# Kernel tuning notes

Measured on AMD Instinct MI355X. Metric: run time of the kernel, lower is better.

Reference implementation:

```python
import jax, jax.numpy as jnp
import numpy as np

NUM_Q = 8
DIM = 256
N_EMBED = 1024
COMMITMENT = 1.0


def setup_inputs() -> dict:
    key = jax.random.key(0)
    kx, ke = jax.random.split(key)
    x = jax.random.normal(kx, (32, 2048, DIM), dtype=jnp.float32)
    # one codebook per residual layer, stored as [dim, n_embed] like torch buffer `embed`
    embeds = jax.random.normal(ke, (NUM_Q, DIM, N_EMBED), dtype=jnp.float32)
    return {"x": x, "embeds": embeds}


def _vq_layer(residual, embed):
    # residual: [B, T, D]; embed: [D, K]
    flat = residual.reshape(-1, DIM)                                   # [N, D]
    dist = (jnp.sum(flat * flat, axis=1, keepdims=True)
            - 2.0 * flat @ embed
            + jnp.sum(embed * embed, axis=0, keepdims=True))           # [N, K]
    ind = jnp.argmin(dist, axis=1)                                     # [N]
    quantize = jnp.take(embed.T, ind, axis=0).reshape(residual.shape)  # [B, T, D]
    # commitment loss: mse(stopgrad(quantize), input)
    loss = jnp.mean((jax.lax.stop_gradient(quantize) - residual) ** 2) * COMMITMENT
    # straight-through estimator
    quantize_st = residual + jax.lax.stop_gradient(quantize - residual)
    # perplexity from code usage histogram
    counts = jnp.zeros((N_EMBED,), dtype=flat.dtype).at[ind].add(1.0)
    avg_probs = counts / flat.shape[0]
    perplexity = jnp.exp(-jnp.sum(avg_probs * jnp.log(avg_probs + 1e-10)))
    return quantize_st, loss, perplexity


def reference(x, embeds):
    def step(carry, embed):
        residual, quantized_out = carry
        q, loss, perp = _vq_layer(residual, embed)
        return (residual - q, quantized_out + q), (loss, perp)

    init = (x, jnp.zeros_like(x))
    (residual, quantized_out), (losses, perps) = jax.lax.scan(step, init, embeds)
    return quantized_out, losses, perps
```

## Files before the change

### kernel.cpp

```cpp
#include <hip/hip_runtime.h>
#include <math.h>
#include <stdint.h>

#define NQ 8
#define DIMV 256
#define KCODES 1024
#define NTOK 65536
#define NELEM (NTOK * DIMV)
#define TOKPB 64

typedef _Float16 f16x8 __attribute__((ext_vector_type(8)));
typedef float    f32x16 __attribute__((ext_vector_type(16)));

__device__ __forceinline__ int rotl3(int s) { return ((s << 3) | (s >> 2)) & 31; }

__global__ __launch_bounds__(256)
void vq_transpose(const float* __restrict__ embeds, float* __restrict__ embedT) {
    const int idx = blockIdx.x * 256 + threadIdx.x;
    const int q   = idx >> 18;
    const int rem = idx & 262143;
    const int k   = rem >> 8;
    const int d   = rem & 255;
    embedT[idx] = embeds[q * 262144 + d * 1024 + k];
}

__global__ __launch_bounds__(256)
void vq_e2(const float* __restrict__ embeds, float* __restrict__ e2) {
    const int idx = blockIdx.x * 256 + threadIdx.x;
    const int q = idx >> 10;
    const int k = idx & 1023;
    const float* e = embeds + q * 262144 + k;
    float s = 0.f;
    for (int d = 0; d < DIMV; ++d) {
        const float v = e[d * 1024];
        s += v * v;
    }
    e2[idx] = s;
}

__global__ __launch_bounds__(256)
void vq_embedB(const float* __restrict__ embeds, _Float16* __restrict__ embedB) {
    const int idx = blockIdx.x * 256 + threadIdx.x;
    const int j    = idx & 7;
    const int s    = (idx >> 3) & 127;
    const int part = (idx >> 10) & 1;
    const int w    = (idx >> 11) & 15;
    const int c    = (idx >> 15) & 15;
    const int q    = idx >> 19;
    const int h  = s >> 6;
    const int cl = s & 63;
    const int d  = c * 16 + h * 8 + j;
    const int k  = w * 64 + cl;
    const float v = embeds[q * 262144 + d * 1024 + k];
    const _Float16 hi = (_Float16)v;
    embedB[idx] = (part == 0) ? hi : (_Float16)(v - (float)hi);
}

#define LDS_BYTES 78272

__global__ __launch_bounds__(1024)
void vq_fused(const float* __restrict__ x, float* __restrict__ out,
              const float* __restrict__ embedT, const float* __restrict__ e2,
              const _Float16* __restrict__ embedB,
              float* __restrict__ lossSum, int* __restrict__ counts) {
    extern __shared__ char smem[];
    _Float16* Ahi = (_Float16*)smem;
    _Float16* Alo = (_Float16*)(smem + 32768);
    float* bestS   = (float*)(smem + 65536);
    int*   bestI   = (int*)(smem + 69696);
    int*   indF    = (int*)(smem + 73856);
    float* lossRed = (float*)(smem + 74112);
    float* e2Lds   = (float*)(smem + 74176);

    const int tid    = threadIdx.x;
    const int wave   = tid >> 6;
    const int lane   = tid & 63;
    const int l32    = lane & 31;
    const int h32    = lane >> 5;
    const int tok0   = blockIdx.x * TOKPB;
    const int codeBase = wave * 64;

#pragma unroll
    for (int k = 0; k < 2; ++k) {
        const int si = tid + k * 1024;
        const int t  = si >> 5;
        const int s  = si & 31;
        const float4 v0 = *(const float4*)(x + (tok0 + t) * 256 + s * 8);
        const float4 v1 = *(const float4*)(x + (tok0 + t) * 256 + s * 8 + 4);
        const float vv[8] = {v0.x, v0.y, v0.z, v0.w, v1.x, v1.y, v1.z, v1.w};
        f16x8 h8, l8;
#pragma unroll
        for (int e = 0; e < 8; ++e) {
            const _Float16 hi = (_Float16)vv[e];
            h8[e] = hi;
            l8[e] = (_Float16)(vv[e] - (float)hi);
        }
        const int ss = rotl3(s) ^ (t & 31);
        ((f16x8*)(Ahi + t * 256))[ss] = h8;
        ((f16x8*)(Alo + t * 256))[ss] = l8;
    }

#pragma unroll 1
    for (int q = 0; q < NQ; ++q) {
        const _Float16* embedBq = embedB + q * 524288;
        const float*    embedTq = embedT + q * (KCODES * DIMV);

        e2Lds[tid] = e2[q * KCODES + tid];
        __syncthreads();

        const char* gBw = (const char*)embedBq + wave * 4096 + h32 * 1024 + l32 * 16;

        float bsv0 = 3.4e38f, bsv1 = 3.4e38f;
        int   biv0 = 0x7fffffff, biv1 = 0x7fffffff;

#pragma unroll
        for (int pass = 0; pass < 2; ++pass) {
            f32x16 acc[2];
#pragma unroll
            for (int tt = 0; tt < 2; ++tt)
#pragma unroll
                for (int r = 0; r < 16; ++r) acc[tt][r] = 0.f;

            const char* gBp = gBw + pass * 512;

            f16x8 bH[3], bL[3];
            bH[0] = *(const f16x8*)(gBp);
            bL[0] = *(const f16x8*)(gBp + 2048);
            bH[1] = *(const f16x8*)(gBp + 65536);
            bL[1] = *(const f16x8*)(gBp + 65536 + 2048);

#pragma unroll
            for (int c = 0; c < 16; ++c) {
                const int cs = c % 3;
                if (c < 14) {
                    const char* gBn = gBp + (c + 2) * 65536;
                    bH[(c + 2) % 3] = *(const f16x8*)(gBn);
                    bL[(c + 2) % 3] = *(const f16x8*)(gBn + 2048);
                }
                f16x8 aH[2], aL[2];
#pragma unroll
                for (int tt = 0; tt < 2; ++tt) {
                    const int t  = tt * 32 + l32;
                    const int ss = rotl3(2 * c + h32) ^ l32;
                    aH[tt] = ((const f16x8*)(Ahi + t * 256))[ss];
                    aL[tt] = ((const f16x8*)(Alo + t * 256))[ss];
                }
#pragma unroll
                for (int tt = 0; tt < 2; ++tt) {
                    acc[tt] = __builtin_amdgcn_mfma_f32_32x32x16_f16(
                        bH[cs], aH[tt], acc[tt], 0, 0, 0);
                    acc[tt] = __builtin_amdgcn_mfma_f32_32x32x16_f16(
                        bL[cs], aH[tt], acc[tt], 0, 0, 0);
                    acc[tt] = __builtin_amdgcn_mfma_f32_32x32x16_f16(
                        bH[cs], aL[tt], acc[tt], 0, 0, 0);
                }
            }

#pragma unroll
            for (int tt = 0; tt < 2; ++tt) {
                float bs = (tt == 0) ? bsv0 : bsv1;
                int   bi = (tt == 0) ? biv0 : biv1;
#pragma unroll
                for (int r = 0; r < 16; ++r) {
                    const int cd = codeBase + pass * 32 + (r & 3) + 8 * (r >> 2) + 4 * h32;
                    const float sc = e2Lds[cd] - 2.0f * acc[tt][r];
                    if (sc < bs || (sc == bs && cd < bi)) { bs = sc; bi = cd; }
                }
                if (tt == 0) { bsv0 = bs; biv0 = bi; } else { bsv1 = bs; biv1 = bi; }
            }
        }

#pragma unroll
        for (int tt = 0; tt < 2; ++tt) {
            float bs = (tt == 0) ? bsv0 : bsv1;
            int   bi = (tt == 0) ? biv0 : biv1;
            const float so = __shfl_xor(bs, 32);
            const int   io = __shfl_xor(bi, 32);
            if (so < bs || (so == bs && io < bi)) { bs = so; bi = io; }
            if (h32 == 0) {
                bestS[wave * 65 + tt * 32 + l32] = bs;
                bestI[wave * 65 + tt * 32 + l32] = bi;
            }
        }
        __syncthreads();

        if (tid < 256) {
            const int t = tid >> 2;
            const int g = tid & 3;
            float bs = 3.4e38f;
            int   bi = 0x7fffffff;
#pragma unroll
            for (int i = 0; i < 4; ++i) {
                const int w = g * 4 + i;
                const float s2 = bestS[w * 65 + t];
                const int   i2 = bestI[w * 65 + t];
                if (s2 < bs || (s2 == bs && i2 < bi)) { bs = s2; bi = i2; }
            }
#pragma unroll
            for (int m = 1; m < 4; m <<= 1) {
                const float so = __shfl_xor(bs, m);
                const int   io = __shfl_xor(bi, m);
                if (so < bs || (so == bs && io < bi)) { bs = so; bi = io; }
            }
            if (g == 0) {
                indF[t] = bi;
                atomicAdd(&counts[q * KCODES + bi], 1);
            }
        }
        __syncthreads();

        {
            const int tl = tid >> 4;
            const int sg = tid & 15;
            const int csel = indF[tl];
            const float* gq = embedTq + csel * 256 + sg * 16;
            float lp = 0.f;
            f16x8* rowH = (f16x8*)(Ahi + tl * 256);
            f16x8* rowL = (f16x8*)(Alo + tl * 256);
#pragma unroll
            for (int it = 0; it < 2; ++it) {
                const int slot = rotl3(sg * 2 + it) ^ (tl & 31);
                f16x8 h8 = rowH[slot];
                f16x8 l8 = rowL[slot];
                const float4 q0 = *(const float4*)(gq + it * 8);
                const float4 q1 = *(const float4*)(gq + it * 8 + 4);
                const float qv[8] = {q0.x, q0.y, q0.z, q0.w, q1.x, q1.y, q1.z, q1.w};
#pragma unroll
                for (int e = 0; e < 8; ++e) {
                    const float rv = (float)h8[e] + (float)l8[e];
                    const float nr = rv - qv[e];
                    lp += nr * nr;
                    const _Float16 nh = (_Float16)nr;
                    h8[e] = nh;
                    l8[e] = (_Float16)(nr - (float)nh);
                }
                rowH[slot] = h8;
                rowL[slot] = l8;
            }
#pragma unroll
            for (int off = 32; off > 0; off >>= 1) lp += __shfl_down(lp, off);
            if (lane == 0) lossRed[wave] = lp;
        }
        __syncthreads();
        if (tid < 64) {
            float v = (lane < 16) ? lossRed[lane] : 0.f;
#pragma unroll
            for (int off = 8; off > 0; off >>= 1) v += __shfl_down(v, off);
            if (lane == 0) atomicAdd(lossSum + q, v);
        }
    }

#pragma unroll
    for (int k = 0; k < 2; ++k) {
        const int si = tid + k * 1024;
        const int t  = si >> 5;
        const int s  = si & 31;
        const int ss = rotl3(s) ^ (t & 31);
        const f16x8 h8 = ((const f16x8*)(Ahi + t * 256))[ss];
        const f16x8 l8 = ((const f16x8*)(Alo + t * 256))[ss];
        const float4 x0 = *(const float4*)(x + (tok0 + t) * 256 + s * 8);
        const float4 x1 = *(const float4*)(x + (tok0 + t) * 256 + s * 8 + 4);
        float4 o0, o1;
        o0.x = x0.x - ((float)h8[0] + (float)l8[0]);
        o0.y = x0.y - ((float)h8[1] + (float)l8[1]);
        o0.z = x0.z - ((float)h8[2] + (float)l8[2]);
        o0.w = x0.w - ((float)h8[3] + (float)l8[3]);
        o1.x = x1.x - ((float)h8[4] + (float)l8[4]);
        o1.y = x1.y - ((float)h8[5] + (float)l8[5]);
        o1.z = x1.z - ((float)h8[6] + (float)l8[6]);
        o1.w = x1.w - ((float)h8[7] + (float)l8[7]);
        *(float4*)(out + (tok0 + t) * 256 + s * 8)     = o0;
        *(float4*)(out + (tok0 + t) * 256 + s * 8 + 4) = o1;
    }
}

__global__ __launch_bounds__(256)
void vq_finalize(const int* __restrict__ counts, const float* __restrict__ lossSum,
                 float* __restrict__ outTail) {
    const int q = blockIdx.x;
    const int tid = threadIdx.x;
    float s = 0.f;
    for (int k = tid; k < KCODES; k += 256) {
        const float p = (float)counts[q * KCODES + k] * (1.0f / 65536.0f);
        s += p * logf(p + 1e-10f);
    }
    for (int off = 32; off > 0; off >>= 1) s += __shfl_down(s, off);
    __shared__ float wpart[4];
    if ((tid & 63) == 0) wpart[tid >> 6] = s;
    __syncthreads();
    if (tid == 0) {
        outTail[q]     = lossSum[q] * (1.0f / 16777216.0f);
        outTail[8 + q] = expf(-(wpart[0] + wpart[1] + wpart[2] + wpart[3]));
    }
}

extern "C" void kernel_launch(void* const* d_in, const int* in_sizes, int n_in,
                              void* d_out, int out_size, void* d_ws, size_t ws_size,
                              hipStream_t stream) {
    const float* x      = (const float*)d_in[0];
    const float* embeds = (const float*)d_in[1];
    float* out = (float*)d_out;

    float* embedT   = (float*)d_ws;
    float* e2       = embedT + 2097152;
    float* lossSum  = e2 + 8192;
    int*   counts   = (int*)(lossSum + 8);
    _Float16* embedB = (_Float16*)(counts + 8192);

    hipMemsetAsync(lossSum, 0, (8 + 8192) * sizeof(float), stream);

    vq_transpose<<<8192, 256, 0, stream>>>(embeds, embedT);
    vq_e2<<<32, 256, 0, stream>>>(embeds, e2);
    vq_embedB<<<16384, 256, 0, stream>>>(embeds, embedB);

    hipFuncSetAttribute((const void*)vq_fused,
                        hipFuncAttributeMaxDynamicSharedMemorySize, LDS_BYTES);
    vq_fused<<<NTOK / TOKPB, 1024, LDS_BYTES, stream>>>(
        x, out, embedT, e2, embedB, lossSum, counts);

    vq_finalize<<<NQ, 256, 0, stream>>>(counts, lossSum, out + NELEM);
}
```

Baseline: 1.421 ms.

## Halve tokens per block and give each wave 128 codes for one token tile

The fused VQ kernel now processes 32 tokens per 512-thread block instead of 64 tokens per 1024-thread block. Each wave scans 128 codes against a single 32-token MFMA tile instead of 64 codes against two tiles, and the LDS layout and reductions are resized to match. The aim is to cut LDS per block and per-wave register pressure so more blocks fit per CU and latency is better hidden. In exchange, each embedding fragment loaded from global memory is reused across half as many tokens, which doubles codebook read traffic.

```diff
diff --git a/kernel.cpp b/kernel.cpp
--- a/kernel.cpp
+++ b/kernel.cpp
@@ -7,7 +7,7 @@
 #define KCODES 1024
 #define NTOK 65536
 #define NELEM (NTOK * DIMV)
-#define TOKPB 64
+#define TOKPB 32
 
 typedef _Float16 f16x8 __attribute__((ext_vector_type(8)));
 typedef float    f32x16 __attribute__((ext_vector_type(16)));
@@ -56,21 +56,21 @@
     embedB[idx] = (part == 0) ? hi : (_Float16)(v - (float)hi);
 }
 
-#define LDS_BYTES 78272
-
-__global__ __launch_bounds__(1024)
+#define LDS_BYTES 39296
+
+__global__ __launch_bounds__(512, 4)
 void vq_fused(const float* __restrict__ x, float* __restrict__ out,
               const float* __restrict__ embedT, const float* __restrict__ e2,
               const _Float16* __restrict__ embedB,
               float* __restrict__ lossSum, int* __restrict__ counts) {
     extern __shared__ char smem[];
     _Float16* Ahi = (_Float16*)smem;
-    _Float16* Alo = (_Float16*)(smem + 32768);
-    float* bestS   = (float*)(smem + 65536);
-    int*   bestI   = (int*)(smem + 69696);
-    int*   indF    = (int*)(smem + 73856);
-    float* lossRed = (float*)(smem + 74112);
-    float* e2Lds   = (float*)(smem + 74176);
+    _Float16* Alo = (_Float16*)(smem + 16384);
+    float* bestS   = (float*)(smem + 32768);
+    int*   bestI   = (int*)(smem + 33888);
+    int*   indF    = (int*)(smem + 35008);
+    float* lossRed = (float*)(smem + 35136);
+    float* e2Lds   = (float*)(smem + 35200);
 
     const int tid    = threadIdx.x;
     const int wave   = tid >> 6;
@@ -78,11 +78,10 @@
     const int l32    = lane & 31;
     const int h32    = lane >> 5;
     const int tok0   = blockIdx.x * TOKPB;
-    const int codeBase = wave * 64;
 
 #pragma unroll
     for (int k = 0; k < 2; ++k) {
-        const int si = tid + k * 1024;
+        const int si = tid + k * 512;
         const int t  = si >> 5;
         const int s  = si & 31;
         const float4 v0 = *(const float4*)(x + (tok0 + t) * 256 + s * 8);
@@ -105,23 +104,21 @@
         const _Float16* embedBq = embedB + q * 524288;
         const float*    embedTq = embedT + q * (KCODES * DIMV);
 
-        e2Lds[tid] = e2[q * KCODES + tid];
-        __syncthreads();
-
-        const char* gBw = (const char*)embedBq + wave * 4096 + h32 * 1024 + l32 * 16;
-
-        float bsv0 = 3.4e38f, bsv1 = 3.4e38f;
-        int   biv0 = 0x7fffffff, biv1 = 0x7fffffff;
-
-#pragma unroll
-        for (int pass = 0; pass < 2; ++pass) {
-            f32x16 acc[2];
-#pragma unroll
-            for (int tt = 0; tt < 2; ++tt)
-#pragma unroll
-                for (int r = 0; r < 16; ++r) acc[tt][r] = 0.f;
-
-            const char* gBp = gBw + pass * 512;
+        e2Lds[tid]       = e2[q * KCODES + tid];
+        e2Lds[tid + 512] = e2[q * KCODES + tid + 512];
+        __syncthreads();
+
+        float bsv = 3.4e38f;
+        int   biv = 0x7fffffff;
+
+#pragma unroll
+        for (int p = 0; p < 4; ++p) {
+            f32x16 acc;
+#pragma unroll
+            for (int r = 0; r < 16; ++r) acc[r] = 0.f;
+
+            const char* gBp = (const char*)embedBq + (2 * wave + (p >> 1)) * 4096
+                              + (p & 1) * 512 + h32 * 1024 + l32 * 16;
 
             f16x8 bH[3], bL[3];
             bH[0] = *(const f16x8*)(gBp);
@@ -137,67 +134,40 @@
                     bH[(c + 2) % 3] = *(const f16x8*)(gBn);
                     bL[(c + 2) % 3] = *(const f16x8*)(gBn + 2048);
                 }
-                f16x8 aH[2], aL[2];
-#pragma unroll
-                for (int tt = 0; tt < 2; ++tt) {
-                    const int t  = tt * 32 + l32;
-                    const int ss = rotl3(2 * c + h32) ^ l32;
-                    aH[tt] = ((const f16x8*)(Ahi + t * 256))[ss];
-                    aL[tt] = ((const f16x8*)(Alo + t * 256))[ss];
-                }
-#pragma unroll
-                for (int tt = 0; tt < 2; ++tt) {
-                    acc[tt] = __builtin_amdgcn_mfma_f32_32x32x16_f16(
-                        bH[cs], aH[tt], acc[tt], 0, 0, 0);
-                    acc[tt] = __builtin_amdgcn_mfma_f32_32x32x16_f16(
-                        bL[cs], aH[tt], acc[tt], 0, 0, 0);
-                    acc[tt] = __builtin_amdgcn_mfma_f32_32x32x16_f16(
-                        bH[cs], aL[tt], acc[tt], 0, 0, 0);
-                }
-            }
-
-#pragma unroll
-            for (int tt = 0; tt < 2; ++tt) {
-                float bs = (tt == 0) ? bsv0 : bsv1;
-                int   bi = (tt == 0) ? biv0 : biv1;
-#pragma unroll
-                for (int r = 0; r < 16; ++r) {
-                    const int cd = codeBase + pass * 32 + (r & 3) + 8 * (r >> 2) + 4 * h32;
-                    const float sc = e2Lds[cd] - 2.0f * acc[tt][r];
-                    if (sc < bs || (sc == bs && cd < bi)) { bs = sc; bi = cd; }
-                }
-                if (tt == 0) { bsv0 = bs; biv0 = bi; } else { bsv1 = bs; biv1 = bi; }
-            }
-        }
-
-#pragma unroll
-        for (int tt = 0; tt < 2; ++tt) {
-            float bs = (tt == 0) ? bsv0 : bsv1;
-            int   bi = (tt == 0) ? biv0 : biv1;
-            const float so = __shfl_xor(bs, 32);
-            const int   io = __shfl_xor(bi, 32);
-            if (so < bs || (so == bs && io < bi)) { bs = so; bi = io; }
+                const int ss = rotl3(2 * c + h32) ^ l32;
+                const f16x8 aH = ((const f16x8*)(Ahi + l32 * 256))[ss];
+                const f16x8 aL = ((const f16x8*)(Alo + l32 * 256))[ss];
+                acc = __builtin_amdgcn_mfma_f32_32x32x16_f16(bH[cs], aH, acc, 0, 0, 0);
+                acc = __builtin_amdgcn_mfma_f32_32x32x16_f16(bL[cs], aH, acc, 0, 0, 0);
+                acc = __builtin_amdgcn_mfma_f32_32x32x16_f16(bH[cs], aL, acc, 0, 0, 0);
+            }
+
+#pragma unroll
+            for (int r = 0; r < 16; ++r) {
+                const int cd = wave * 128 + p * 32 + (r & 3) + 8 * (r >> 2) + 4 * h32;
+                const float sc = e2Lds[cd] - 2.0f * acc[r];
+                if (sc < bsv || (sc == bsv && cd < biv)) { bsv = sc; biv = cd; }
+            }
+        }
+
+        {
+            const float so = __shfl_xor(bsv, 32);
+            const int   io = __shfl_xor(biv, 32);
+            if (so < bsv || (so == bsv && io < biv)) { bsv = so; biv = io; }
             if (h32 == 0) {
-                bestS[wave * 65 + tt * 32 + l32] = bs;
-                bestI[wave * 65 + tt * 32 + l32] = bi;
+                bestS[wave * 35 + l32] = bsv;
+                bestI[wave * 35 + l32] = biv;
             }
         }
         __syncthreads();
 
         if (tid < 256) {
-            const int t = tid >> 2;
-            const int g = tid & 3;
-            float bs = 3.4e38f;
-            int   bi = 0x7fffffff;
-#pragma unroll
-            for (int i = 0; i < 4; ++i) {
-                const int w = g * 4 + i;
-                const float s2 = bestS[w * 65 + t];
-                const int   i2 = bestI[w * 65 + t];
-                if (s2 < bs || (s2 == bs && i2 < bi)) { bs = s2; bi = i2; }
-            }
-#pragma unroll
-            for (int m = 1; m < 4; m <<= 1) {
+            const int t = tid >> 3;
+            const int g = tid & 7;
+            float bs = bestS[g * 35 + t];
+            int   bi = bestI[g * 35 + t];
+#pragma unroll
+            for (int m = 1; m < 8; m <<= 1) {
                 const float so = __shfl_xor(bs, m);
                 const int   io = __shfl_xor(bi, m);
                 if (so < bs || (so == bs && io < bi)) { bs = so; bi = io; }
@@ -243,16 +213,16 @@
         }
         __syncthreads();
         if (tid < 64) {
-            float v = (lane < 16) ? lossRed[lane] : 0.f;
-#pragma unroll
-            for (int off = 8; off > 0; off >>= 1) v += __shfl_down(v, off);
+            float v = (lane < 8) ? lossRed[lane] : 0.f;
+#pragma unroll
+            for (int off = 4; off > 0; off >>= 1) v += __shfl_down(v, off);
             if (lane == 0) atomicAdd(lossSum + q, v);
         }
     }
 
 #pragma unroll
     for (int k = 0; k < 2; ++k) {
-        const int si = tid + k * 1024;
+        const int si = tid + k * 512;
         const int t  = si >> 5;
         const int s  = si & 31;
         const int ss = rotl3(s) ^ (t & 31);
@@ -315,7 +285,7 @@
 
     hipFuncSetAttribute((const void*)vq_fused,
                         hipFuncAttributeMaxDynamicSharedMemorySize, LDS_BYTES);
-    vq_fused<<<NTOK / TOKPB, 1024, LDS_BYTES, stream>>>(
+    vq_fused<<<NTOK / TOKPB, 512, LDS_BYTES, stream>>>(
         x, out, embedT, e2, embedB, lossSum, counts);
 
     vq_finalize<<<NQ, 256, 0, stream>>>(counts, lossSum, out + NELEM);
```

New measurement: 2.940 ms. 107% more time.
